# Optimization experiments

Hardware: AMD Instinct MI355X
Metric: run time of the kernel (lower is better)

Reference implementation:

```python
import jax, jax.numpy as jnp
import numpy as np
from jax import lax

N, D, M, H = 8192, 32, 8, 128
ATOL = 1e-5
RTOL = 1e-5
MAX_STEPS = 10   # bounded adaptive dopri5 iterations (accept/reject with masking)
DT0 = 0.25


def setup_inputs() -> dict:
    key = jax.random.key(0)
    ks = jax.random.split(key, 6)
    p = lambda k, shape, s: jax.random.normal(k, shape, jnp.float32) * s
    return {
        "z": jax.random.normal(ks[0], (N, D), jnp.float32),
        "G_w": p(ks[1], (M, D), 0.3),
        "W1": p(ks[2], (H, D), (1.0 / D) ** 0.5),
        "b1": jnp.zeros((H,), jnp.float32),
        "W2": p(ks[3], (H, H), (1.0 / H) ** 0.5),
        "b2": jnp.zeros((H,), jnp.float32),
        "W3": p(ks[4], (D, H), (1.0 / H) ** 0.5),
        "b3": jnp.zeros((D,), jnp.float32),
        "T": jnp.ones((1,), jnp.float32),
    }


def qpnf_forward(z, G_w, W1, b1, W2, b2, W3, b3, T):
    d = z.shape[1]

    def mlp(x):  # dF network: d -> 128 -> 128 -> d
        h = jax.nn.relu(x @ W1.T + b1)
        h = jax.nn.relu(h @ W2.T + b2)
        return h @ W3.T + b3

    # G is linear (no bias) so jacrev(G)(x) == G_w for every sample; the batched
    # dG @ dG^T solves collapse to one shared (m,m) solve / (d,d) projector.
    A = G_w @ G_w.T                       # (m, m)
    AinvG = jnp.linalg.solve(A, G_w)      # (m, d) = A^{-1} W
    P = G_w.T @ AinvG                     # (d, d) null-space projector W^T A^{-1} W
    IP = jnp.eye(d, dtype=z.dtype) - P
    trP = jnp.trace(P)

    jac_mlp = jax.vmap(jax.jacrev(lambda xi: mlp(xi[None, :])[0]))  # (N,d,d)

    def f(y):  # augmented state y = [x | logp], dlogp/dt = -div(dx/dx)
        x = y[:, :d]
        dF = mlp(x)                        # (N, d)
        g = x @ G_w.T                      # (N, m)
        dz = -(dF @ IP) - g @ AinvG        # -(eta_J) - (eta_C)
        JdF = jac_mlp(x)                   # (N, d, d)
        # J_f = -(I-P) JdF - P  ->  dlogp = -trace(J_f)
        dlogp = jnp.einsum('jk,nkj->n', IP, JdF) + trP
        return jnp.concatenate([dz, dlogp[:, None]], axis=1)

    def rk_step(y, dt):  # Dormand-Prince 5(4)
        k1 = f(y)
        k2 = f(y + dt * (0.2 * k1))
        k3 = f(y + dt * (3/40 * k1 + 9/40 * k2))
        k4 = f(y + dt * (44/45 * k1 - 56/15 * k2 + 32/9 * k3))
        k5 = f(y + dt * (19372/6561 * k1 - 25360/2187 * k2 + 64448/6561 * k3 - 212/729 * k4))
        k6 = f(y + dt * (9017/3168 * k1 - 355/33 * k2 + 46732/5247 * k3 + 49/176 * k4 - 5103/18656 * k5))
        y1 = y + dt * (35/384 * k1 + 500/1113 * k3 + 125/192 * k4 - 2187/6784 * k5 + 11/84 * k6)
        k7 = f(y1)
        err = dt * ((35/384 - 5179/57600) * k1 + (500/1113 - 7571/16695) * k3
                    + (125/192 - 393/640) * k4 + (-2187/6784 + 92097/339200) * k5
                    + (11/84 - 187/2100) * k6 - (1/40) * k7)
        return y1, err

    t1 = 2.0 * T[0]  # eval path: integration_times[-1] *= 2
    y0 = jnp.concatenate([z, jnp.zeros((z.shape[0], 1), z.dtype)], axis=1)

    def body(carry, _):
        t, dt, y = carry
        done = t >= t1 - 1e-9
        dtc = jnp.where(done, jnp.asarray(1e-3, z.dtype), jnp.minimum(dt, t1 - t))
        y1, ev = rk_step(y, dtc)
        tol = ATOL + RTOL * jnp.maximum(jnp.abs(y), jnp.abs(y1))
        errn = jnp.sqrt(jnp.mean((ev / tol) ** 2))
        accept = jnp.logical_and(~done, errn <= 1.0)
        y_new = jnp.where(accept, y1, y)
        t_new = jnp.where(accept, t + dtc, t)
        factor = jnp.clip(0.9 * errn ** (-0.2), 0.2, 10.0)
        dt_new = jnp.where(done, dt, jnp.clip(dtc * factor, 1e-6, t1))
        dt_new = lax.stop_gradient(dt_new)
        return (t_new, dt_new, y_new), None

    init = (jnp.asarray(0.0, z.dtype), jnp.asarray(DT0, z.dtype), y0)
    (_, _, yT), _ = lax.scan(body, init, None, length=MAX_STEPS)
    return yT[:, :d]


def reference(z, G_w, W1, b1, W2, b2, W3, b3, T):
    return qpnf_forward(z, G_w, W1, b1, W2, b2, W3, b3, T)
```

## Files before the change

### kernel.cpp

```cpp
#include <hip/hip_runtime.h>
#include <hip/hip_cooperative_groups.h>
#include <math.h>

namespace cg = cooperative_groups;
typedef float4 f4;

#define NT 512
#define RB 32

#define WS_WR    0
#define WS_PART  32768
#define WS_TOTAL 35328

#define L_W1T   0
#define L_C3T   4096
#define L_P     8320
#define L_PT    9344
#define L_HST   10496
#define L_HS2   15104
#define L_XST   19712
#define L_B1    20864
#define L_B2    20992
#define L_C0    21120
#define L_GS    21152
#define L_AAUG  21408
#define L_AINVG 21536
#define L_MISC  21792
#define L_KZ    21796
#define L_KL    29860
#define L_YZ    30084
#define L_Y1Z   31236
#define L_YL    32388
#define L_Y1L   32420
#define LDS_FLOATS 32452
#define L_RED   L_XST

__device__ const float ACO[5][5] = {
  { 0.2f, 0.f, 0.f, 0.f, 0.f },
  { (float)(3.0/40.0), (float)(9.0/40.0), 0.f, 0.f, 0.f },
  { (float)(44.0/45.0), (float)(-56.0/15.0), (float)(32.0/9.0), 0.f, 0.f },
  { (float)(19372.0/6561.0), (float)(-25360.0/2187.0), (float)(64448.0/6561.0), (float)(-212.0/729.0), 0.f },
  { (float)(9017.0/3168.0), (float)(-355.0/33.0), (float)(46732.0/5247.0), (float)(49.0/176.0), (float)(-5103.0/18656.0) }
};

#define B1C ((float)(35.0/384.0))
#define B3C ((float)(500.0/1113.0))
#define B4C ((float)(125.0/192.0))
#define B5C ((float)(-2187.0/6784.0))
#define B6C ((float)(11.0/84.0))

#define E1C ((float)(35.0/384.0 - 5179.0/57600.0))
#define E3C ((float)(500.0/1113.0 - 7571.0/16695.0))
#define E4C ((float)(125.0/192.0 - 393.0/640.0))
#define E5C ((float)(-2187.0/6784.0 + 92097.0/339200.0))
#define E6C ((float)(11.0/84.0 - 187.0/2100.0))
#define E7C ((float)(-1.0/40.0))

__device__ __forceinline__ f4 ld4(const float* p){ return *(const f4*)p; }
__device__ __forceinline__ void st4(float* p, f4 v){ *(f4*)p = v; }

__device__ void assemble_x(float* lds, int tid, float dtc, const float* co, int np)
{
  __syncthreads();
  if (tid < 256){
    const int r = tid >> 3, jj = (tid & 7) * 4;
    const int o = r * 36 + jj;
    f4 y = ld4(&lds[L_YZ + o]);
    float sx = 0.f, sy = 0.f, sz = 0.f, sw = 0.f;
    for (int p = 0; p < np; p++){
      f4 kv = ld4(&lds[L_KZ + p * 1152 + o]);
      float c = co[p];
      sx += c * kv.x; sy += c * kv.y; sz += c * kv.z; sw += c * kv.w;
    }
    lds[L_XST + (jj + 0) * 36 + r] = y.x + dtc * sx;
    lds[L_XST + (jj + 1) * 36 + r] = y.y + dtc * sy;
    lds[L_XST + (jj + 2) * 36 + r] = y.z + dtc * sz;
    lds[L_XST + (jj + 3) * 36 + r] = y.w + dtc * sw;
  }
  __syncthreads();
}

__device__ void eval_f(float* lds, const float* __restrict__ ws, int tid,
                       float trP, int kout)
{
  const int cg = tid & 31, kh = (tid >> 5) & 1, wv = tid >> 6;
  const int row4 = 4 * wv;

  float a1[4][4];
#pragma unroll
  for (int i = 0; i < 4; i++)
#pragma unroll
    for (int j = 0; j < 4; j++) a1[i][j] = 0.f;
#pragma unroll 4
  for (int t = 0; t < 16; t++){
    const int k = kh * 16 + t;
    f4 av = ld4(&lds[L_XST + k * 36 + row4]);
    f4 bv = ld4(&lds[L_W1T + k * 128 + 4 * cg]);
    const float* ap = (const float*)&av;
    const float* bp = (const float*)&bv;
#pragma unroll
    for (int i = 0; i < 4; i++)
#pragma unroll
      for (int j = 0; j < 4; j++) a1[i][j] += bp[i] * ap[j];
  }
#pragma unroll
  for (int i = 0; i < 4; i++)
#pragma unroll
    for (int j = 0; j < 4; j++) a1[i][j] += __shfl_xor(a1[i][j], 32);
  if (kh == 0){
    f4 b1v = ld4(&lds[L_B1 + 4 * cg]);
    const float* b1p = (const float*)&b1v;
#pragma unroll
    for (int i = 0; i < 4; i++){
      f4 hv; float* hp = (float*)&hv;
#pragma unroll
      for (int j = 0; j < 4; j++) hp[j] = fmaxf(a1[i][j] + b1p[i], 0.f);
      st4(&lds[L_HST + (4 * cg + i) * 36 + row4], hv);
    }
  }
  __syncthreads();

  float ah[4][4], at[4][4];
#pragma unroll
  for (int i = 0; i < 4; i++)
#pragma unroll
    for (int j = 0; j < 4; j++){ ah[i][j] = 0.f; at[i][j] = 0.f; }
  const f4* WR4 = (const f4*)&ws[WS_WR];
  const int kb = kh * 64;
  f4 wb[4], rb[4];
#pragma unroll
  for (int u = 0; u < 4; u++){
    wb[u] = WR4[(kb + u) * 64 + cg];
    rb[u] = WR4[(kb + u) * 64 + 32 + cg];
  }
#pragma unroll 1
  for (int g = 0; g < 16; g++){
    f4 wc[4], rc[4];
#pragma unroll
    for (int u = 0; u < 4; u++){ wc[u] = wb[u]; rc[u] = rb[u]; }
    if (g < 15){
      const int kn = kb + (g + 1) * 4;
#pragma unroll
      for (int u = 0; u < 4; u++){
        wb[u] = WR4[(kn + u) * 64 + cg];
        rb[u] = WR4[(kn + u) * 64 + 32 + cg];
      }
    }
#pragma unroll
    for (int u = 0; u < 4; u++){
      const int k = kb + g * 4 + u;
      f4 av = ld4(&lds[L_HST + k * 36 + row4]);
      const float* ap = (const float*)&av;
      const float* wp = (const float*)&wc[u];
      const float* rp = (const float*)&rc[u];
      float m[4];
#pragma unroll
      for (int j = 0; j < 4; j++) m[j] = (ap[j] > 0.f) ? 1.f : 0.f;
#pragma unroll
      for (int i = 0; i < 4; i++)
#pragma unroll
        for (int j = 0; j < 4; j++){
          ah[i][j] += wp[i] * ap[j];
          at[i][j] += rp[i] * m[j];
        }
    }
  }
#pragma unroll
  for (int i = 0; i < 4; i++)
#pragma unroll
    for (int j = 0; j < 4; j++){
      ah[i][j] += __shfl_xor(ah[i][j], 32);
      at[i][j] += __shfl_xor(at[i][j], 32);
    }

  f4 b2v = ld4(&lds[L_B2 + 4 * cg]);
  const float* b2p = (const float*)&b2v;
  float h2v[4][4]; float dl[4] = {0.f, 0.f, 0.f, 0.f};
#pragma unroll
  for (int i = 0; i < 4; i++)
#pragma unroll
    for (int j = 0; j < 4; j++){
      float pre = ah[i][j] + b2p[i];
      float hv = fmaxf(pre, 0.f);
      h2v[i][j] = hv;
      if (pre > 0.f) dl[j] += at[i][j];
    }
#pragma unroll
  for (int mk = 1; mk < 32; mk <<= 1){
#pragma unroll
    for (int j = 0; j < 4; j++) dl[j] += __shfl_xor(dl[j], mk, 64);
  }
  if (kh == 0){
#pragma unroll
    for (int i = 0; i < 4; i++){
      f4 hv; float* hp = (float*)&hv;
#pragma unroll
      for (int j = 0; j < 4; j++) hp[j] = h2v[i][j];
      st4(&lds[L_HS2 + (4 * cg + i) * 36 + row4], hv);
    }
    if (cg == 0){
#pragma unroll
      for (int j = 0; j < 4; j++)
        lds[L_KL + kout * 32 + row4 + j] = dl[j] + trP;
    }
  }
  __syncthreads();

  float a3[4] = {0.f, 0.f, 0.f, 0.f};
  const int bb = kh * 64;
#pragma unroll 4
  for (int t = 0; t < 16; t++){
    f4 cv = ld4(&lds[L_C3T + cg * 132 + bb + 4 * t]);
    const float* cp = (const float*)&cv;
#pragma unroll
    for (int u = 0; u < 4; u++){
      f4 av = ld4(&lds[L_HS2 + (bb + 4 * t + u) * 36 + row4]);
      const float* ap = (const float*)&av;
#pragma unroll
      for (int j = 0; j < 4; j++) a3[j] += ap[j] * cp[u];
    }
  }
  const int qq = kh * 16;
#pragma unroll
  for (int t = 0; t < 4; t++){
    f4 pv = ld4(&lds[L_PT + cg * 36 + qq + 4 * t]);
    const float* pp = (const float*)&pv;
#pragma unroll
    for (int u = 0; u < 4; u++){
      f4 av = ld4(&lds[L_XST + (qq + 4 * t + u) * 36 + row4]);
      const float* ap = (const float*)&av;
#pragma unroll
      for (int j = 0; j < 4; j++) a3[j] += ap[j] * pp[u];
    }
  }
#pragma unroll
  for (int j = 0; j < 4; j++) a3[j] += __shfl_xor(a3[j], 32);
  if (kh == 0){
    float c0v = lds[L_C0 + cg];
#pragma unroll
    for (int j = 0; j < 4; j++)
      lds[L_KZ + kout * 1152 + (row4 + j) * 36 + cg] = -(a3[j] + c0v);
  }
}

__global__ void __launch_bounds__(NT, 2)
qpnf_kernel(const float* __restrict__ z, const float* __restrict__ Gw,
            const float* __restrict__ W1g, const float* __restrict__ b1g,
            const float* __restrict__ W2g, const float* __restrict__ b2g,
            const float* __restrict__ W3g, const float* __restrict__ b3g,
            const float* __restrict__ Tg, float* __restrict__ out,
            float* __restrict__ ws)
{
  __shared__ float lds[LDS_FLOATS];
  const int tid = threadIdx.x;
  const int bid = blockIdx.x;
  const int r0 = bid * RB;
  cg::grid_group grid = cg::this_grid();

  for (int i = 0; i < 8; i++){
    int idx = tid + i * NT;
    int h = idx >> 5, j = idx & 31;
    lds[L_W1T + j * 128 + h] = W1g[idx];
  }
  if (tid < 128){ lds[L_B1 + tid] = b1g[tid]; lds[L_B2 + tid] = b2g[tid]; }
  if (tid < 256) lds[L_GS + tid] = Gw[tid];
  __syncthreads();

  if (tid < 64){
    int i = tid >> 3, j = tid & 7;
    float s = 0.f;
    for (int k = 0; k < 32; k++) s += lds[L_GS + i * 32 + k] * lds[L_GS + j * 32 + k];
    lds[L_AAUG + i * 16 + j] = s;
    lds[L_AAUG + i * 16 + 8 + j] = (i == j) ? 1.f : 0.f;
  }
  __syncthreads();
  if (tid == 0){
    float* A = &lds[L_AAUG];
    for (int c = 0; c < 8; c++){
      int p = c; float mx = fabsf(A[c * 16 + c]);
      for (int r = c + 1; r < 8; r++){
        float v = fabsf(A[r * 16 + c]);
        if (v > mx){ mx = v; p = r; }
      }
      if (p != c)
        for (int q = 0; q < 16; q++){ float t = A[c*16+q]; A[c*16+q] = A[p*16+q]; A[p*16+q] = t; }
      float pv = 1.0f / A[c * 16 + c];
      for (int q = 0; q < 16; q++) A[c * 16 + q] *= pv;
      for (int r = 0; r < 8; r++) if (r != c){
        float fct = A[r * 16 + c];
        for (int q = 0; q < 16; q++) A[r * 16 + q] -= fct * A[c * 16 + q];
      }
    }
  }
  __syncthreads();
  if (tid < 256){
    int m = tid >> 5, d = tid & 31;
    float s = 0.f;
    for (int q = 0; q < 8; q++) s += lds[L_AAUG + m * 16 + 8 + q] * lds[L_GS + q * 32 + d];
    lds[L_AINVG + m * 32 + d] = s;
  }
  __syncthreads();
  for (int i4 = 0; i4 < 2; i4++){
    int idx = tid + i4 * NT;
    int i = idx >> 5, j = idx & 31;
    float s = 0.f;
    for (int m = 0; m < 8; m++) s += lds[L_GS + m * 32 + i] * lds[L_AINVG + m * 32 + j];
    lds[L_P + i * 32 + j] = s;
  }
  __syncthreads();
  float* IPl = &lds[L_XST];
  for (int i4 = 0; i4 < 2; i4++){
    int idx = tid + i4 * NT;
    int i = idx >> 5, j = idx & 31;
    IPl[i * 32 + j] = ((i == j) ? 1.f : 0.f) - lds[L_P + i * 32 + j];
  }
  if (tid == 0){
    float s = 0.f;
    for (int i = 0; i < 32; i++) s += lds[L_P + i * 32 + i];
    lds[L_MISC] = s;
  }
  __syncthreads();
  for (int i4 = 0; i4 < 8; i4++){
    int idx = tid + i4 * NT;
    int b = idx & 127, c = idx >> 7;
    float s = 0.f;
    for (int i = 0; i < 32; i++) s += W3g[i * 128 + b] * IPl[i * 32 + c];
    lds[L_C3T + c * 132 + b] = s;
  }
  for (int i4 = 0; i4 < 2; i4++){
    int idx = tid + i4 * NT;
    int c = idx >> 5, q = idx & 31;
    lds[L_PT + c * 36 + q] = lds[L_P + q * 32 + c];
  }
  if (tid < 32){
    float s = 0.f;
    for (int i = 0; i < 32; i++) s += b3g[i] * IPl[i * 32 + tid];
    lds[L_C0 + tid] = s;
  }
  for (int i4 = 0; i4 < 8; i4++){
    int idx = tid + i4 * NT;
    int j = idx >> 7, b = idx & 127;
    float s = 0.f;
    for (int k = 0; k < 32; k++) s += IPl[j * 32 + k] * W3g[k * 128 + b];
    lds[L_HST + j * 128 + b] = s;
  }
  __syncthreads();
  if (bid < 128 && tid < 128){
    int a = bid;
    float s = 0.f;
    for (int j = 0; j < 32; j++) s += W1g[a * 32 + j] * lds[L_HST + j * 128 + tid];
    ws[WS_WR + a * 256 + 128 + tid] = s * W2g[tid * 128 + a];
  }
  if (bid >= 128 && tid < 128){
    int a = bid - 128;
    ws[WS_WR + a * 256 + tid] = W2g[tid * 128 + a];
  }
  if (tid < 256){
    const int r = tid >> 3, jj = (tid & 7) * 4;
    st4(&lds[L_YZ + r * 36 + jj], ld4(&z[(r0 + r) * 32 + jj]));
  }
  if (tid < RB) lds[L_YL + tid] = 0.f;

  const float trP = lds[L_MISC];
  const float t1 = 2.0f * Tg[0];

  grid.sync();

  float t_cur = 0.f, dt_cur = 0.25f;
  bool prev_acc = false;

  for (int step = 0; step < 10; step++){
    if (t_cur >= t1 - 1e-9f) break;
    const float dtc = fminf(dt_cur, t1 - t_cur);

    for (int s = 1; s <= 6; s++){
      if (s == 1 && step > 0){
        if (prev_acc){
          if (tid < 256){
            const int r = tid >> 3, jj = (tid & 7) * 4;
            const int o = r * 36 + jj;
            st4(&lds[L_KZ + o], ld4(&lds[L_KZ + 6 * 1152 + o]));
          }
          if (tid < RB) lds[L_KL + tid] = lds[L_KL + 6 * 32 + tid];
        }
        continue;
      }
      assemble_x(lds, tid, dtc, ACO[s >= 2 ? s - 2 : 0], s - 1);
      eval_f(lds, ws, tid, trP, s - 1);
    }

    __syncthreads();
    if (tid < 256){
      const int r = tid >> 3, jj = (tid & 7) * 4;
      const int o = r * 36 + jj;
      f4 y   = ld4(&lds[L_YZ + o]);
      f4 k1v = ld4(&lds[L_KZ + 0 * 1152 + o]);
      f4 k3v = ld4(&lds[L_KZ + 2 * 1152 + o]);
      f4 k4v = ld4(&lds[L_KZ + 3 * 1152 + o]);
      f4 k5v = ld4(&lds[L_KZ + 4 * 1152 + o]);
      f4 k6v = ld4(&lds[L_KZ + 5 * 1152 + o]);
      f4 x;
      x.x = y.x + dtc * (B1C*k1v.x + B3C*k3v.x + B4C*k4v.x + B5C*k5v.x + B6C*k6v.x);
      x.y = y.y + dtc * (B1C*k1v.y + B3C*k3v.y + B4C*k4v.y + B5C*k5v.y + B6C*k6v.y);
      x.z = y.z + dtc * (B1C*k1v.z + B3C*k3v.z + B4C*k4v.z + B5C*k5v.z + B6C*k6v.z);
      x.w = y.w + dtc * (B1C*k1v.w + B3C*k3v.w + B4C*k4v.w + B5C*k5v.w + B6C*k6v.w);
      st4(&lds[L_Y1Z + o], x);
      lds[L_XST + (jj + 0) * 36 + r] = x.x;
      lds[L_XST + (jj + 1) * 36 + r] = x.y;
      lds[L_XST + (jj + 2) * 36 + r] = x.z;
      lds[L_XST + (jj + 3) * 36 + r] = x.w;
    }
    if (tid < RB){
      float s = B1C * lds[L_KL + 0*32 + tid] + B3C * lds[L_KL + 2*32 + tid]
              + B4C * lds[L_KL + 3*32 + tid] + B5C * lds[L_KL + 4*32 + tid]
              + B6C * lds[L_KL + 5*32 + tid];
      lds[L_Y1L + tid] = lds[L_YL + tid] + dtc * s;
    }
    __syncthreads();
    eval_f(lds, ws, tid, trP, 6);
    __syncthreads();

    float sacc = 0.f;
    if (tid < 256){
      const int r = tid >> 3, jj = (tid & 7) * 4;
      const int o = r * 36 + jj;
      f4 k1v = ld4(&lds[L_KZ + 0 * 1152 + o]);
      f4 k3v = ld4(&lds[L_KZ + 2 * 1152 + o]);
      f4 k4v = ld4(&lds[L_KZ + 3 * 1152 + o]);
      f4 k5v = ld4(&lds[L_KZ + 4 * 1152 + o]);
      f4 k6v = ld4(&lds[L_KZ + 5 * 1152 + o]);
      f4 k7v = ld4(&lds[L_KZ + 6 * 1152 + o]);
      f4 yv  = ld4(&lds[L_YZ + o]);
      f4 y1v = ld4(&lds[L_Y1Z + o]);
      float ev, tol, q;
      ev = dtc * (E1C*k1v.x + E3C*k3v.x + E4C*k4v.x + E5C*k5v.x + E6C*k6v.x + E7C*k7v.x);
      tol = 1e-5f + 1e-5f * fmaxf(fabsf(yv.x), fabsf(y1v.x)); q = ev / tol; sacc += q * q;
      ev = dtc * (E1C*k1v.y + E3C*k3v.y + E4C*k4v.y + E5C*k5v.y + E6C*k6v.y + E7C*k7v.y);
      tol = 1e-5f + 1e-5f * fmaxf(fabsf(yv.y), fabsf(y1v.y)); q = ev / tol; sacc += q * q;
      ev = dtc * (E1C*k1v.z + E3C*k3v.z + E4C*k4v.z + E5C*k5v.z + E6C*k6v.z + E7C*k7v.z);
      tol = 1e-5f + 1e-5f * fmaxf(fabsf(yv.z), fabsf(y1v.z)); q = ev / tol; sacc += q * q;
      ev = dtc * (E1C*k1v.w + E3C*k3v.w + E4C*k4v.w + E5C*k5v.w + E6C*k6v.w + E7C*k7v.w);
      tol = 1e-5f + 1e-5f * fmaxf(fabsf(yv.w), fabsf(y1v.w)); q = ev / tol; sacc += q * q;
    }
    if (tid < RB){
      float evl = dtc * (E1C * lds[L_KL + 0*32 + tid] + E3C * lds[L_KL + 2*32 + tid]
                + E4C * lds[L_KL + 3*32 + tid] + E5C * lds[L_KL + 4*32 + tid]
                + E6C * lds[L_KL + 5*32 + tid] + E7C * lds[L_KL + 6*32 + tid]);
      float toll = 1e-5f + 1e-5f * fmaxf(fabsf(lds[L_YL + tid]), fabsf(lds[L_Y1L + tid]));
      float ql = evl / toll; sacc += ql * ql;
    }
    __syncthreads();
    lds[L_RED + tid] = sacc; __syncthreads();
    for (int o = 256; o > 0; o >>= 1){
      if (tid < o) lds[L_RED + tid] += lds[L_RED + tid + o];
      __syncthreads();
    }
    if (tid == 0) ws[WS_PART + step * 256 + bid] = lds[L_RED + 0];

    grid.sync();

    if (tid < 256) lds[L_RED + tid] = ws[WS_PART + step * 256 + tid];
    __syncthreads();
    for (int o = 128; o > 0; o >>= 1){
      if (tid < o) lds[L_RED + tid] += lds[L_RED + tid + o];
      __syncthreads();
    }
    const float errn = sqrtf(lds[L_RED + 0] / 270336.0f);
    __syncthreads();

    const bool accept = (errn <= 1.0f);
    if (accept){
      if (tid < 256){
        const int r = tid >> 3, jj = (tid & 7) * 4;
        const int o = r * 36 + jj;
        st4(&lds[L_YZ + o], ld4(&lds[L_Y1Z + o]));
      }
      if (tid < RB) lds[L_YL + tid] = lds[L_Y1L + tid];
      t_cur += dtc;
    }
    float fac = 0.9f * powf(errn, -0.2f);
    fac = fminf(fmaxf(fac, 0.2f), 10.0f);
    dt_cur = fminf(fmaxf(dtc * fac, 1e-6f), t1);
    prev_acc = accept;
  }

  __syncthreads();
  if (tid < 256){
    const int r = tid >> 3, jj = (tid & 7) * 4;
    st4(&out[(r0 + r) * 32 + jj], ld4(&lds[L_YZ + r * 36 + jj]));
  }
}

extern "C" void kernel_launch(void* const* d_in, const int* in_sizes, int n_in,
                              void* d_out, int out_size, void* d_ws, size_t ws_size,
                              hipStream_t stream)
{
  (void)in_sizes; (void)n_in; (void)out_size;
  const float* z  = (const float*)d_in[0];
  const float* Gw = (const float*)d_in[1];
  const float* W1 = (const float*)d_in[2];
  const float* b1 = (const float*)d_in[3];
  const float* W2 = (const float*)d_in[4];
  const float* b2 = (const float*)d_in[5];
  const float* W3 = (const float*)d_in[6];
  const float* b3 = (const float*)d_in[7];
  const float* T  = (const float*)d_in[8];
  float* out = (float*)d_out;
  float* ws  = (float*)d_ws;
  if (ws_size < (size_t)WS_TOTAL * sizeof(float)) return;

  void* args[] = { (void*)&z, (void*)&Gw, (void*)&W1, (void*)&b1, (void*)&W2,
                   (void*)&b2, (void*)&W3, (void*)&b3, (void*)&T, (void*)&out,
                   (void*)&ws };
  hipLaunchCooperativeKernel((const void*)qpnf_kernel, dim3(256), dim3(NT),
                             args, 0, stream);
}
```

Before: 1.300 ms.

## Double block size to 1024 threads and repartition MLP work across waves

Raises the threads per block from 512 to 1024 and remaps the eval_f work so each wave covers a half of the hidden columns with a 4-way K split, reduced through extra cross-lane shuffles. The divergence partial sums are combined across the two column halves through a small LDS buffer. The block error reduction now uses wave shuffles plus a 16-entry LDS pass instead of a tree of __syncthreads. The aim is more latency hiding per block on the 32-row tile, at the cost of extra shuffle reductions, higher register pressure from launch_bounds(1024,4), and added barriers.

```diff
diff --git a/kernel.cpp b/kernel.cpp
--- a/kernel.cpp
+++ b/kernel.cpp
@@ -5,7 +5,7 @@
 namespace cg = cooperative_groups;
 typedef float4 f4;
 
-#define NT 512
+#define NT 1024
 #define RB 32
 
 #define WS_WR    0
@@ -32,7 +32,9 @@
 #define L_Y1Z   31236
 #define L_YL    32388
 #define L_Y1L   32420
-#define LDS_FLOATS 32452
+#define L_DLP   32452
+#define L_RED16 32516
+#define LDS_FLOATS 32532
 #define L_RED   L_XST
 
 __device__ const float ACO[5][5] = {
@@ -83,19 +85,22 @@
 __device__ void eval_f(float* lds, const float* __restrict__ ws, int tid,
                        float trP, int kout)
 {
-  const int cg = tid & 31, kh = (tid >> 5) & 1, wv = tid >> 6;
-  const int row4 = 4 * wv;
+  const int lane = tid & 63, w = tid >> 6;
+  const int cg = lane & 15, kh = lane >> 4;
+  const int rw = w & 7, ch = w >> 3;
+  const int row4 = 4 * rw;
+  const int col4 = ch * 64 + 4 * cg;
 
   float a1[4][4];
 #pragma unroll
   for (int i = 0; i < 4; i++)
 #pragma unroll
     for (int j = 0; j < 4; j++) a1[i][j] = 0.f;
-#pragma unroll 4
-  for (int t = 0; t < 16; t++){
-    const int k = kh * 16 + t;
+#pragma unroll
+  for (int t = 0; t < 8; t++){
+    const int k = kh * 8 + t;
     f4 av = ld4(&lds[L_XST + k * 36 + row4]);
-    f4 bv = ld4(&lds[L_W1T + k * 128 + 4 * cg]);
+    f4 bv = ld4(&lds[L_W1T + k * 128 + col4]);
     const float* ap = (const float*)&av;
     const float* bp = (const float*)&bv;
 #pragma unroll
@@ -106,16 +111,19 @@
 #pragma unroll
   for (int i = 0; i < 4; i++)
 #pragma unroll
-    for (int j = 0; j < 4; j++) a1[i][j] += __shfl_xor(a1[i][j], 32);
+    for (int j = 0; j < 4; j++){
+      a1[i][j] += __shfl_xor(a1[i][j], 16);
+      a1[i][j] += __shfl_xor(a1[i][j], 32);
+    }
   if (kh == 0){
-    f4 b1v = ld4(&lds[L_B1 + 4 * cg]);
+    f4 b1v = ld4(&lds[L_B1 + col4]);
     const float* b1p = (const float*)&b1v;
 #pragma unroll
     for (int i = 0; i < 4; i++){
       f4 hv; float* hp = (float*)&hv;
 #pragma unroll
       for (int j = 0; j < 4; j++) hp[j] = fmaxf(a1[i][j] + b1p[i], 0.f);
-      st4(&lds[L_HST + (4 * cg + i) * 36 + row4], hv);
+      st4(&lds[L_HST + (col4 + i) * 36 + row4], hv);
     }
   }
   __syncthreads();
@@ -126,24 +134,25 @@
 #pragma unroll
     for (int j = 0; j < 4; j++){ ah[i][j] = 0.f; at[i][j] = 0.f; }
   const f4* WR4 = (const f4*)&ws[WS_WR];
-  const int kb = kh * 64;
+  const int kb = kh * 32;
+  const int wcol = ch * 16 + cg;
   f4 wb[4], rb[4];
 #pragma unroll
   for (int u = 0; u < 4; u++){
-    wb[u] = WR4[(kb + u) * 64 + cg];
-    rb[u] = WR4[(kb + u) * 64 + 32 + cg];
+    wb[u] = WR4[(kb + u) * 64 + wcol];
+    rb[u] = WR4[(kb + u) * 64 + 32 + wcol];
   }
 #pragma unroll 1
-  for (int g = 0; g < 16; g++){
+  for (int g = 0; g < 8; g++){
     f4 wc[4], rc[4];
 #pragma unroll
     for (int u = 0; u < 4; u++){ wc[u] = wb[u]; rc[u] = rb[u]; }
-    if (g < 15){
+    if (g < 7){
       const int kn = kb + (g + 1) * 4;
 #pragma unroll
       for (int u = 0; u < 4; u++){
-        wb[u] = WR4[(kn + u) * 64 + cg];
-        rb[u] = WR4[(kn + u) * 64 + 32 + cg];
+        wb[u] = WR4[(kn + u) * 64 + wcol];
+        rb[u] = WR4[(kn + u) * 64 + 32 + wcol];
       }
     }
 #pragma unroll
@@ -169,11 +178,13 @@
   for (int i = 0; i < 4; i++)
 #pragma unroll
     for (int j = 0; j < 4; j++){
+      ah[i][j] += __shfl_xor(ah[i][j], 16);
       ah[i][j] += __shfl_xor(ah[i][j], 32);
+      at[i][j] += __shfl_xor(at[i][j], 16);
       at[i][j] += __shfl_xor(at[i][j], 32);
     }
 
-  f4 b2v = ld4(&lds[L_B2 + 4 * cg]);
+  f4 b2v = ld4(&lds[L_B2 + col4]);
   const float* b2p = (const float*)&b2v;
   float h2v[4][4]; float dl[4] = {0.f, 0.f, 0.f, 0.f};
 #pragma unroll
@@ -186,9 +197,9 @@
       if (pre > 0.f) dl[j] += at[i][j];
     }
 #pragma unroll
-  for (int mk = 1; mk < 32; mk <<= 1){
-#pragma unroll
-    for (int j = 0; j < 4; j++) dl[j] += __shfl_xor(dl[j], mk, 64);
+  for (int mk = 1; mk < 16; mk <<= 1){
+#pragma unroll
+    for (int j = 0; j < 4; j++) dl[j] += __shfl_xor(dl[j], mk);
   }
   if (kh == 0){
 #pragma unroll
@@ -196,21 +207,27 @@
       f4 hv; float* hp = (float*)&hv;
 #pragma unroll
       for (int j = 0; j < 4; j++) hp[j] = h2v[i][j];
-      st4(&lds[L_HS2 + (4 * cg + i) * 36 + row4], hv);
+      st4(&lds[L_HS2 + (col4 + i) * 36 + row4], hv);
     }
     if (cg == 0){
 #pragma unroll
-      for (int j = 0; j < 4; j++)
-        lds[L_KL + kout * 32 + row4 + j] = dl[j] + trP;
-    }
-  }
-  __syncthreads();
-
+      for (int j = 0; j < 4; j++) lds[L_DLP + w * 4 + j] = dl[j];
+    }
+  }
+  __syncthreads();
+
+  if (tid < 32){
+    const int rw2 = tid >> 2, j = tid & 3;
+    lds[L_KL + kout * 32 + tid] =
+        lds[L_DLP + rw2 * 4 + j] + lds[L_DLP + (8 + rw2) * 4 + j] + trP;
+  }
+
+  const int cc = ch * 16 + cg;
   float a3[4] = {0.f, 0.f, 0.f, 0.f};
-  const int bb = kh * 64;
+  const int bb = kh * 32;
 #pragma unroll 4
-  for (int t = 0; t < 16; t++){
-    f4 cv = ld4(&lds[L_C3T + cg * 132 + bb + 4 * t]);
+  for (int t = 0; t < 8; t++){
+    f4 cv = ld4(&lds[L_C3T + cc * 132 + bb + 4 * t]);
     const float* cp = (const float*)&cv;
 #pragma unroll
     for (int u = 0; u < 4; u++){
@@ -220,10 +237,10 @@
       for (int j = 0; j < 4; j++) a3[j] += ap[j] * cp[u];
     }
   }
-  const int qq = kh * 16;
-#pragma unroll
-  for (int t = 0; t < 4; t++){
-    f4 pv = ld4(&lds[L_PT + cg * 36 + qq + 4 * t]);
+  const int qq = kh * 8;
+#pragma unroll
+  for (int t = 0; t < 2; t++){
+    f4 pv = ld4(&lds[L_PT + cc * 36 + qq + 4 * t]);
     const float* pp = (const float*)&pv;
 #pragma unroll
     for (int u = 0; u < 4; u++){
@@ -234,16 +251,19 @@
     }
   }
 #pragma unroll
-  for (int j = 0; j < 4; j++) a3[j] += __shfl_xor(a3[j], 32);
+  for (int j = 0; j < 4; j++){
+    a3[j] += __shfl_xor(a3[j], 16);
+    a3[j] += __shfl_xor(a3[j], 32);
+  }
   if (kh == 0){
-    float c0v = lds[L_C0 + cg];
+    float c0v = lds[L_C0 + cc];
 #pragma unroll
     for (int j = 0; j < 4; j++)
-      lds[L_KZ + kout * 1152 + (row4 + j) * 36 + cg] = -(a3[j] + c0v);
+      lds[L_KZ + kout * 1152 + (row4 + j) * 36 + cc] = -(a3[j] + c0v);
   }
 }
 
-__global__ void __launch_bounds__(NT, 2)
+__global__ void __launch_bounds__(NT, 4)
 qpnf_kernel(const float* __restrict__ z, const float* __restrict__ Gw,
             const float* __restrict__ W1g, const float* __restrict__ b1g,
             const float* __restrict__ W2g, const float* __restrict__ b2g,
@@ -257,7 +277,7 @@
   const int r0 = bid * RB;
   cg::grid_group grid = cg::this_grid();
 
-  for (int i = 0; i < 8; i++){
+  for (int i = 0; i < 4; i++){
     int idx = tid + i * NT;
     int h = idx >> 5, j = idx & 31;
     lds[L_W1T + j * 128 + h] = W1g[idx];
@@ -300,18 +320,16 @@
     lds[L_AINVG + m * 32 + d] = s;
   }
   __syncthreads();
-  for (int i4 = 0; i4 < 2; i4++){
-    int idx = tid + i4 * NT;
-    int i = idx >> 5, j = idx & 31;
+  {
+    int i = tid >> 5, j = tid & 31;
     float s = 0.f;
     for (int m = 0; m < 8; m++) s += lds[L_GS + m * 32 + i] * lds[L_AINVG + m * 32 + j];
     lds[L_P + i * 32 + j] = s;
   }
   __syncthreads();
   float* IPl = &lds[L_XST];
-  for (int i4 = 0; i4 < 2; i4++){
-    int idx = tid + i4 * NT;
-    int i = idx >> 5, j = idx & 31;
+  {
+    int i = tid >> 5, j = tid & 31;
     IPl[i * 32 + j] = ((i == j) ? 1.f : 0.f) - lds[L_P + i * 32 + j];
   }
   if (tid == 0){
@@ -320,16 +338,15 @@
     lds[L_MISC] = s;
   }
   __syncthreads();
-  for (int i4 = 0; i4 < 8; i4++){
+  for (int i4 = 0; i4 < 4; i4++){
     int idx = tid + i4 * NT;
     int b = idx & 127, c = idx >> 7;
     float s = 0.f;
     for (int i = 0; i < 32; i++) s += W3g[i * 128 + b] * IPl[i * 32 + c];
     lds[L_C3T + c * 132 + b] = s;
   }
-  for (int i4 = 0; i4 < 2; i4++){
-    int idx = tid + i4 * NT;
-    int c = idx >> 5, q = idx & 31;
+  {
+    int c = tid >> 5, q = tid & 31;
     lds[L_PT + c * 36 + q] = lds[L_P + q * 32 + c];
   }
   if (tid < 32){
@@ -337,7 +354,7 @@
     for (int i = 0; i < 32; i++) s += b3g[i] * IPl[i * 32 + tid];
     lds[L_C0 + tid] = s;
   }
-  for (int i4 = 0; i4 < 8; i4++){
+  for (int i4 = 0; i4 < 4; i4++){
     int idx = tid + i4 * NT;
     int j = idx >> 7, b = idx & 127;
     float s = 0.f;
@@ -361,6 +378,7 @@
   }
   if (tid < RB) lds[L_YL + tid] = 0.f;
 
+  __syncthreads();
   const float trP = lds[L_MISC];
   const float t1 = 2.0f * Tg[0];
 
@@ -449,14 +467,15 @@
       float toll = 1e-5f + 1e-5f * fmaxf(fabsf(lds[L_YL + tid]), fabsf(lds[L_Y1L + tid]));
       float ql = evl / toll; sacc += ql * ql;
     }
-    __syncthreads();
-    lds[L_RED + tid] = sacc; __syncthreads();
-    for (int o = 256; o > 0; o >>= 1){
-      if (tid < o) lds[L_RED + tid] += lds[L_RED + tid + o];
-      __syncthreads();
-    }
-    if (tid == 0) ws[WS_PART + step * 256 + bid] = lds[L_RED + 0];
-
+#pragma unroll
+    for (int mk = 1; mk < 64; mk <<= 1) sacc += __shfl_xor(sacc, mk);
+    if ((tid & 63) == 0) lds[L_RED16 + (tid >> 6)] = sacc;
+    __syncthreads();
+    if (tid == 0){
+      float s = 0.f;
+      for (int i = 0; i < 16; i++) s += lds[L_RED16 + i];
+      ws[WS_PART + step * 256 + bid] = s;
+    }
     grid.sync();
 
     if (tid < 256) lds[L_RED + tid] = ws[WS_PART + step * 256 + tid];
@@ -482,6 +501,7 @@
     fac = fminf(fmaxf(fac, 0.2f), 10.0f);
     dt_cur = fminf(fmaxf(dtc * fac, 1e-6f), t1);
     prev_acc = accept;
+    __syncthreads();
   }
 
   __syncthreads();
```

Result: slower. 1.935 ms (+48.9%).
